# Performance work log

Measured on AMD Instinct MI355X. Metric: run time of the kernel, lower is better.

## Reference

```python
import jax, jax.numpy as jnp
import numpy as np

DIM = 128


def setup_inputs() -> dict:
    key = jax.random.key(0)
    k1, k2, k3, k4 = jax.random.split(key, 4)
    x = jax.random.normal(k1, (8, 32768, DIM), dtype=jnp.float32)
    # nn.Linear(dim, dim*3, bias=False): weight applied as x @ W.T; store as [dim, 3*dim]
    W_qkv = jax.random.normal(k2, (DIM, 3 * DIM), dtype=jnp.float32) * (DIM ** -0.5)
    W_out = jax.random.normal(k3, (DIM, DIM), dtype=jnp.float32) * (DIM ** -0.5)
    b_out = jax.random.normal(k4, (DIM,), dtype=jnp.float32) * 0.01
    return {"x": x, "W_qkv": W_qkv, "W_out": W_out, "b_out": b_out}


def reference(x, W_qkv, W_out, b_out):
    dim = x.shape[-1]
    scale = dim ** -0.5
    qkv = x @ W_qkv  # [b, n, 3d]
    q, k, v = jnp.split(qkv, 3, axis=-1)
    q = jax.nn.softmax(q, axis=-1) * scale
    k = jax.nn.softmax(k, axis=-1)
    v = jax.nn.softmax(v, axis=-1)
    context = jnp.einsum('bnd,bne->bde', q, k)  # [b, d, d]
    out = jnp.einsum('bde,bne->bnd', context, v)  # [b, n, d]
    return out @ W_out + b_out
```

## Files before the change

kernel.cpp:

```cpp
#include <hip/hip_runtime.h>

#define SEQ 32768
#define QSCALE 0.08838834764831845f
#define NCH 16

typedef __attribute__((ext_vector_type(8))) short short8;
typedef __attribute__((ext_vector_type(8))) __bf16 bf16x8;
typedef __attribute__((ext_vector_type(16))) float f32x16;
typedef __attribute__((ext_vector_type(4))) float f32x4;
typedef __attribute__((ext_vector_type(2))) float f32x2;
typedef __attribute__((ext_vector_type(4))) int int4v;
typedef __attribute__((ext_vector_type(2))) int int2v;

#define SWZ(r, c) ((((r) << 7) + (c)) ^ (((r) & 15) << 3))
#define PSWZ(ch, n) ((((ch) << 6) + (n)) ^ (((ch) & 7) << 3))

__device__ __forceinline__ int cvtpk(float lo, float hi) {
  int r;
  asm("v_cvt_pk_bf16_f32 %0, %1, %2" : "=v"(r) : "v"(lo), "v"(hi));
  return r;
}

__device__ __forceinline__ short bf16b(float f) {
  unsigned u = __builtin_bit_cast(unsigned, f);
  u += 0x7fffu + ((u >> 16) & 1u);
  return (short)(u >> 16);
}

__device__ __forceinline__ f32x16 mfma_ii(int4v a, int4v b, f32x16 c) {
  return __builtin_amdgcn_mfma_f32_32x32x16_bf16(
      __builtin_bit_cast(bf16x8, a), __builtin_bit_cast(bf16x8, b), c, 0, 0, 0);
}

__device__ __forceinline__ int4v build_frag(float e0, float e1, float e2, float e3,
                                            float e4, float e5, float e6, float e7,
                                            int hi) {
  int t0 = cvtpk(e0, e1), t1 = cvtpk(e2, e3);
  int t2 = cvtpk(e4, e5), t3 = cvtpk(e6, e7);
  const int u0 = __shfl_xor(t2, 32), u1 = __shfl_xor(t3, 32);
  const int u2 = __shfl_xor(t0, 32), u3 = __shfl_xor(t1, 32);
  int4v f;
  f[0] = hi ? u0 : t0;
  f[1] = hi ? u1 : t1;
  f[2] = hi ? t2 : u2;
  f[3] = hi ? t3 : u3;
  return f;
}

__global__ void la_prep(const float* __restrict__ Wqkv, int4v* __restrict__ Wf) {
  const int fid = blockIdx.x * 256 + threadIdx.x;
  if (fid >= 6144) return;
  const int side = fid >> 11;
  const int rem = fid & 2047;
  const int tile = rem >> 9;
  const int ks = (rem >> 6) & 7;
  const int lane = rem & 63;
  const int k0 = ks * 16 + ((lane >> 5) << 3);
  const int col = side * 128 + tile * 32 + (lane & 31);
  int4v f;
  #pragma unroll
  for (int a = 0; a < 4; ++a)
    f[a] = cvtpk(Wqkv[(k0 + 2 * a) * 384 + col], Wqkv[(k0 + 2 * a + 1) * 384 + col]);
  Wf[fid] = f;
}

__global__ __launch_bounds__(1024, 4)
void la_pass1(const float* __restrict__ x, const int4v* __restrict__ Wf,
              float* __restrict__ partials) {
  __shared__ __align__(16) short xs[2][64 * 128];
  __shared__ __align__(16) short ptile[2][2][128 * 64];
  __shared__ __align__(16) float sumbuf[2][2][2][32][4];

  const int tid = threadIdx.x;
  const int lane = tid & 63;
  const int wv = tid >> 6;
  const int l31 = lane & 31;
  const int hi = lane >> 5;
  const int koff = hi << 3;
  const int h = wv >> 3;
  const int c = (wv >> 1) & 3;
  const int rh = wv & 1;
  const int td = wv >> 2;
  const int te = wv & 3;
  const int b = blockIdx.x >> 5;
  const int strip = blockIdx.x & 31;
  const long base = (long)b * SEQ + (long)strip * (NCH * 64);

  int4v wf[8];
  #pragma unroll
  for (int ks = 0; ks < 8; ++ks)
    wf[ks] = Wf[((((h << 2) + c) << 3) + ks) * 64 + lane];

  const int lr = tid >> 4;
  const int cf = (tid & 15) << 3;
  {
    const float* xp = x + (base + lr) * 128 + cf;
    f32x4 u0 = *(const f32x4*)xp;
    f32x4 u1 = *(const f32x4*)(xp + 4);
    int4v p;
    p[0] = cvtpk(u0[0], u0[1]); p[1] = cvtpk(u0[2], u0[3]);
    p[2] = cvtpk(u1[0], u1[1]); p[3] = cvtpk(u1[2], u1[3]);
    *(int4v*)&xs[0][SWZ(lr, cf)] = p;
  }
  __syncthreads();

  f32x16 ctx = {0.f};
  const int r0 = rh << 5;
  for (int i = 0; i < NCH; ++i) {
    const int cur = i & 1;
    const int inx = (i + 1 < NCH) ? i + 1 : i;
    const float* xp = x + (base + inx * 64 + lr) * 128 + cf;
    f32x4 u0 = *(const f32x4*)xp;
    f32x4 u1 = *(const f32x4*)(xp + 4);

    f32x16 acc = {0.f};
    #pragma unroll
    for (int ks = 0; ks < 8; ++ks) {
      const int4v xf = *(const int4v*)&xs[cur][SWZ(r0 + l31, (ks << 4) + koff)];
      acc = mfma_ii(wf[ks], xf, acc);
    }
    {
      float sa = 0.f, sb = 0.f;
      #pragma unroll
      for (int r = 0; r < 16; r += 2) {
        acc[r] = __expf(acc[r]);         sa += acc[r];
        acc[r + 1] = __expf(acc[r + 1]); sb += acc[r + 1];
      }
      float s = sa + sb;
      s += __shfl_xor(s, 32);
      if (!hi) sumbuf[cur][h][rh][l31][c] = s;
    }

    {
      int4v p;
      p[0] = cvtpk(u0[0], u0[1]); p[1] = cvtpk(u0[2], u0[3]);
      p[2] = cvtpk(u1[0], u1[1]); p[3] = cvtpk(u1[2], u1[3]);
      *(int4v*)&xs[cur ^ 1][SWZ(lr, cf)] = p;
    }
    __syncthreads();

    if (i > 0) {
      const int pb = cur ^ 1;
      #pragma unroll
      for (int ks = 0; ks < 4; ++ks) {
        const int4v aq = *(const int4v*)&ptile[pb][0][PSWZ((td << 5) + l31, (ks << 4) + koff)];
        const int4v bk = *(const int4v*)&ptile[pb][1][PSWZ((te << 5) + l31, (ks << 4) + koff)];
        ctx = mfma_ii(aq, bk, ctx);
      }
    }

    {
      short* pt = &ptile[cur][h][0];
      const int n = (rh << 5) + l31;
      if (h == 0) {
        const f32x4 sq = *(const f32x4*)&sumbuf[cur][0][rh][l31][0];
        const f32x4 sk = *(const f32x4*)&sumbuf[cur][1][rh][l31][0];
        const float invn = QSCALE * __builtin_amdgcn_rcpf(
            (sq[0] + sq[1] + sq[2] + sq[3]) * (sk[0] + sk[1] + sk[2] + sk[3]));
        #pragma unroll
        for (int r = 0; r < 16; ++r) {
          const int ch = (c << 5) + (r & 3) + ((r >> 2) << 3) + (hi << 2);
          pt[PSWZ(ch, n)] = bf16b(acc[r] * invn);
        }
      } else {
        #pragma unroll
        for (int r = 0; r < 16; ++r) {
          const int ch = (c << 5) + (r & 3) + ((r >> 2) << 3) + (hi << 2);
          pt[PSWZ(ch, n)] = bf16b(acc[r]);
        }
      }
    }
  }
  __syncthreads();
  {
    const int pb = (NCH - 1) & 1;
    #pragma unroll
    for (int ks = 0; ks < 4; ++ks) {
      const int4v aq = *(const int4v*)&ptile[pb][0][PSWZ((td << 5) + l31, (ks << 4) + koff)];
      const int4v bk = *(const int4v*)&ptile[pb][1][PSWZ((te << 5) + l31, (ks << 4) + koff)];
      ctx = mfma_ii(aq, bk, ctx);
    }
  }

  float* pout = partials + (long)blockIdx.x * 16384;
  #pragma unroll
  for (int r = 0; r < 16; ++r) {
    const int drow = (td << 5) + (r & 3) + ((r >> 2) << 3) + (hi << 2);
    pout[(drow << 7) + (te << 5) + l31] = ctx[r];
  }
}

__global__ __launch_bounds__(1024, 1)
void la_rm(const float* __restrict__ partials, const float* __restrict__ Wout,
           int4v* __restrict__ Mtf, int strips) {
  __shared__ __align__(16) float cl[128 * 68];
  __shared__ __align__(16) float wo[128 * 128];

  const int tid = threadIdx.x;
  const int b = blockIdx.x >> 1;
  const int eh = blockIdx.x & 1;
  const int ebase = eh << 6;

  #pragma unroll
  for (int t = 0; t < 2; ++t) {
    const int flat = t * 4096 + tid * 4;
    const int d = flat >> 6;
    const int e = flat & 63;
    const long gidx = ((long)d << 7) + ebase + e;
    f32x4 acc = {0.f};
    for (int st = 0; st < strips; ++st)
      acc += *(const f32x4*)(partials + (((long)(b * strips + st)) << 14) + gidx);
    *(f32x4*)&cl[d * 68 + e] = acc;
  }
  #pragma unroll
  for (int t = 0; t < 4; ++t) {
    const int i = t * 4096 + tid * 4;
    *(f32x4*)&wo[i] = *(const f32x4*)(Wout + i);
  }
  __syncthreads();

  const int dq = tid >> 3;
  const int e0 = (tid & 7) << 3;
  float acc[8];
  #pragma unroll
  for (int i = 0; i < 8; ++i) acc[i] = 0.f;
  for (int d = 0; d < 128; ++d) {
    const float w = wo[(d << 7) + dq];
    const float* cr = &cl[d * 68 + e0];
    #pragma unroll
    for (int i = 0; i < 8; ++i) acc[i] += cr[i] * w;
  }

  const int e0g = ebase + e0;
  const int half = dq >> 6, jj = dq & 1, ll = (dq >> 1) & 31;
  const int ks = e0g >> 4, sub = (e0g >> 3) & 1;
  int4v pk;
  pk[0] = cvtpk(acc[0], acc[1]);
  pk[1] = cvtpk(acc[2], acc[3]);
  pk[2] = cvtpk(acc[4], acc[5]);
  pk[3] = cvtpk(acc[6], acc[7]);
  int4v* dst = Mtf + (long)b * 2048 + half * 1024 + jj * 512 + ks * 64;
  dst[sub * 32 + ll] = pk;
}

__global__ __launch_bounds__(256, 4)
void la_pass2(const float* __restrict__ x, const int4v* __restrict__ Wf,
              const int4v* __restrict__ Mtf, const float* __restrict__ bout,
              float* __restrict__ out) {
  __shared__ __align__(16) short xs[4][32 * 128];

  const int tid = threadIdx.x;
  const int lane = tid & 63;
  const int wv = tid >> 6;
  const int l31 = lane & 31;
  const int hi = lane >> 5;
  const int koff = hi << 3;
  const int b = blockIdx.x >> 8;
  const int chunk = blockIdx.x & 255;
  const long row0 = (long)b * SEQ + (long)chunk * 128 + (wv << 5);

  {
    const float* xb = x + row0 * 128;
    f32x4 uA[8];
    #pragma unroll
    for (int t = 0; t < 8; ++t)
      uA[t] = *(const f32x4*)(xb + t * 256 + lane * 4);
    f32x4 uB[8];
    #pragma unroll
    for (int t = 0; t < 8; ++t)
      uB[t] = *(const f32x4*)(xb + (t + 8) * 256 + lane * 4);
    #pragma unroll
    for (int t = 0; t < 8; ++t) {
      const int flat = t * 256 + lane * 4;
      int2v w;
      w[0] = cvtpk(uA[t][0], uA[t][1]);
      w[1] = cvtpk(uA[t][2], uA[t][3]);
      *(int2v*)&xs[wv][SWZ(flat >> 7, flat & 127)] = w;
    }
    #pragma unroll
    for (int t = 0; t < 8; ++t) {
      const int flat = (t + 8) * 256 + lane * 4;
      int2v w;
      w[0] = cvtpk(uB[t][0], uB[t][1]);
      w[1] = cvtpk(uB[t][2], uB[t][3]);
      *(int2v*)&xs[wv][SWZ(flat >> 7, flat & 127)] = w;
    }
  }
  const f32x2 bA = *(const f32x2*)(bout + (l31 << 1));
  const f32x2 bB = *(const f32x2*)(bout + 64 + (l31 << 1));
  asm volatile("s_waitcnt lgkmcnt(0)" ::: "memory");
  __builtin_amdgcn_sched_barrier(0);

  int4v xfr[8];
  #pragma unroll
  for (int ks = 0; ks < 8; ++ks)
    xfr[ks] = *(const int4v*)&xs[wv][SWZ(l31, (ks << 4) + koff)];

  const int4v* WvT = Wf + 2 * 2048;
  f32x16 a0 = {0.f}, a1 = {0.f}, a2 = {0.f}, a3 = {0.f};
  #pragma unroll
  for (int ks = 0; ks < 8; ++ks) {
    a0 = mfma_ii(WvT[(0 * 8 + ks) * 64 + lane], xfr[ks], a0);
    a1 = mfma_ii(WvT[(1 * 8 + ks) * 64 + lane], xfr[ks], a1);
    a2 = mfma_ii(WvT[(2 * 8 + ks) * 64 + lane], xfr[ks], a2);
    a3 = mfma_ii(WvT[(3 * 8 + ks) * 64 + lane], xfr[ks], a3);
  }

  float s = 0.f;
  #pragma unroll
  for (int r = 0; r < 16; ++r) {
    a0[r] = __expf(a0[r]); s += a0[r];
    a1[r] = __expf(a1[r]); s += a1[r];
    a2[r] = __expf(a2[r]); s += a2[r];
    a3[r] = __expf(a3[r]); s += a3[r];
  }
  s += __shfl_xor(s, 32);
  const float inv = __builtin_amdgcn_rcpf(s);
  #pragma unroll
  for (int r = 0; r < 16; ++r) {
    a0[r] *= inv; a1[r] *= inv; a2[r] *= inv; a3[r] *= inv;
  }

  const int4v* MtB = Mtf + ((long)b << 11);
  float* obase = out + row0 * 128 + (l31 << 1);
#define OUT_T2(BASE, T, AT, O0, O1)                                            \
  {                                                                            \
    const int4v f0 = build_frag(AT[0], AT[1], AT[2], AT[3],                    \
                                AT[4], AT[5], AT[6], AT[7], hi);               \
    O0 = mfma_ii(f0, MtB[(BASE) + (2 * T) * 64 + lane], O0);                   \
    O1 = mfma_ii(f0, MtB[(BASE) + 512 + (2 * T) * 64 + lane], O1);             \
    const int4v f1 = build_frag(AT[8], AT[9], AT[10], AT[11],                  \
                                AT[12], AT[13], AT[14], AT[15], hi);           \
    O0 = mfma_ii(f1, MtB[(BASE) + (2 * T + 1) * 64 + lane], O0);               \
    O1 = mfma_ii(f1, MtB[(BASE) + 512 + (2 * T + 1) * 64 + lane], O1);         \
  }
  {
    f32x16 o0 = {0.f}, o1 = {0.f};
    OUT_T2(0, 0, a0, o0, o1)
    OUT_T2(0, 1, a1, o0, o1)
    OUT_T2(0, 2, a2, o0, o1)
    OUT_T2(0, 3, a3, o0, o1)
    #pragma unroll
    for (int r = 0; r < 16; ++r) {
      const int n = (r & 3) + ((r >> 2) << 3) + (hi << 2);
      f32x2 v;
      v[0] = o0[r] + bA[0];
      v[1] = o1[r] + bA[1];
      *(f32x2*)(obase + (long)n * 128) = v;
    }
  }
  {
    f32x16 o2 = {0.f}, o3 = {0.f};
    OUT_T2(1024, 0, a0, o2, o3)
    OUT_T2(1024, 1, a1, o2, o3)
    OUT_T2(1024, 2, a2, o2, o3)
    OUT_T2(1024, 3, a3, o2, o3)
    #pragma unroll
    for (int r = 0; r < 16; ++r) {
      const int n = (r & 3) + ((r >> 2) << 3) + (hi << 2);
      f32x2 v;
      v[0] = o2[r] + bB[0];
      v[1] = o3[r] + bB[1];
      *(f32x2*)(obase + 64 + (long)n * 128) = v;
    }
  }
#undef OUT_T2
}

extern "C" void kernel_launch(void* const* d_in, const int* in_sizes, int n_in,
                              void* d_out, int out_size, void* d_ws, size_t ws_size,
                              hipStream_t stream) {
  const float* x = (const float*)d_in[0];
  const float* Wqkv = (const float*)d_in[1];
  const float* Wout = (const float*)d_in[2];
  const float* bout = (const float*)d_in[3];
  float* out = (float*)d_out;

  const int strips = 32;

  float* partials = (float*)d_ws;
  int4v* Mtf = (int4v*)(partials + (size_t)8 * strips * 16384);
  int4v* Wf = Mtf + 16384;

  la_prep<<<dim3(24), dim3(256), 0, stream>>>(Wqkv, Wf);
  la_pass1<<<dim3(8 * strips), dim3(1024), 0, stream>>>(x, Wf, partials);
  la_rm<<<dim3(16), dim3(1024), 0, stream>>>(partials, Wout, Mtf, strips);
  la_pass2<<<dim3(2048), dim3(256), 0, stream>>>(x, Wf, Mtf, bout, out);
}
```

Before: 144.3 us.

## Compute transposed projection via second MFMA and store prebuilt fragments in LDS

Each wave now runs a second MFMA with swapped operands to get the projection in transposed layout. That layout can be packed straight into MFMA operand fragments with build_frag and stored as whole int4v vectors in LDS, replacing sixteen scattered 16-bit swizzled stores per lane. The original orientation is still computed for the softmax row sums, and the per-row normalisation moves to cross-lane shuffles. This doubles the projection MFMA work to remove the scalar LDS scatter and the bf16 rounding arithmetic in the inner loop.

Result: slower. 157.8 us (+9.3%).

```diff
diff --git a/kernel.cpp b/kernel.cpp
--- a/kernel.cpp
+++ b/kernel.cpp
@@ -13,18 +13,11 @@
 typedef __attribute__((ext_vector_type(2))) int int2v;
 
 #define SWZ(r, c) ((((r) << 7) + (c)) ^ (((r) & 15) << 3))
-#define PSWZ(ch, n) ((((ch) << 6) + (n)) ^ (((ch) & 7) << 3))
 
 __device__ __forceinline__ int cvtpk(float lo, float hi) {
   int r;
   asm("v_cvt_pk_bf16_f32 %0, %1, %2" : "=v"(r) : "v"(lo), "v"(hi));
   return r;
-}
-
-__device__ __forceinline__ short bf16b(float f) {
-  unsigned u = __builtin_bit_cast(unsigned, f);
-  u += 0x7fffu + ((u >> 16) & 1u);
-  return (short)(u >> 16);
 }
 
 __device__ __forceinline__ f32x16 mfma_ii(int4v a, int4v b, f32x16 c) {
@@ -68,7 +61,7 @@
 void la_pass1(const float* __restrict__ x, const int4v* __restrict__ Wf,
               float* __restrict__ partials) {
   __shared__ __align__(16) short xs[2][64 * 128];
-  __shared__ __align__(16) short ptile[2][2][128 * 64];
+  __shared__ int4v fragbuf[2][2][4][4][64];
   __shared__ __align__(16) float sumbuf[2][2][2][32][4];
 
   const int tid = threadIdx.x;
@@ -113,23 +106,26 @@
     f32x4 u0 = *(const f32x4*)xp;
     f32x4 u1 = *(const f32x4*)(xp + 4);
 
-    f32x16 acc = {0.f};
+    f32x16 p2 = {0.f}, p1 = {0.f};
     #pragma unroll
     for (int ks = 0; ks < 8; ++ks) {
       const int4v xf = *(const int4v*)&xs[cur][SWZ(r0 + l31, (ks << 4) + koff)];
-      acc = mfma_ii(wf[ks], xf, acc);
+      p2 = mfma_ii(wf[ks], xf, p2);
+      p1 = mfma_ii(xf, wf[ks], p1);
     }
     {
       float sa = 0.f, sb = 0.f;
       #pragma unroll
       for (int r = 0; r < 16; r += 2) {
-        acc[r] = __expf(acc[r]);         sa += acc[r];
-        acc[r + 1] = __expf(acc[r + 1]); sb += acc[r + 1];
+        sa += __expf(p2[r]);
+        sb += __expf(p2[r + 1]);
       }
       float s = sa + sb;
       s += __shfl_xor(s, 32);
       if (!hi) sumbuf[cur][h][rh][l31][c] = s;
     }
+    #pragma unroll
+    for (int r = 0; r < 16; ++r) p1[r] = __expf(p1[r]);
 
     {
       int4v p;
@@ -142,44 +138,32 @@
     if (i > 0) {
       const int pb = cur ^ 1;
       #pragma unroll
-      for (int ks = 0; ks < 4; ++ks) {
-        const int4v aq = *(const int4v*)&ptile[pb][0][PSWZ((td << 5) + l31, (ks << 4) + koff)];
-        const int4v bk = *(const int4v*)&ptile[pb][1][PSWZ((te << 5) + l31, (ks << 4) + koff)];
-        ctx = mfma_ii(aq, bk, ctx);
+      for (int ks = 0; ks < 4; ++ks)
+        ctx = mfma_ii(fragbuf[pb][0][td][ks][lane], fragbuf[pb][1][te][ks][lane], ctx);
+    }
+
+    if (h == 0) {
+      const f32x4 sq = *(const f32x4*)&sumbuf[cur][0][rh][l31][0];
+      const f32x4 sk = *(const f32x4*)&sumbuf[cur][1][rh][l31][0];
+      const float invn = QSCALE * __builtin_amdgcn_rcpf(
+          (sq[0] + sq[1] + sq[2] + sq[3]) * (sk[0] + sk[1] + sk[2] + sk[3]));
+      #pragma unroll
+      for (int r = 0; r < 16; ++r) {
+        const int nsrc = (r & 3) + ((r >> 2) << 3) + (hi << 2);
+        p1[r] *= __shfl(invn, nsrc);
       }
     }
-
-    {
-      short* pt = &ptile[cur][h][0];
-      const int n = (rh << 5) + l31;
-      if (h == 0) {
-        const f32x4 sq = *(const f32x4*)&sumbuf[cur][0][rh][l31][0];
-        const f32x4 sk = *(const f32x4*)&sumbuf[cur][1][rh][l31][0];
-        const float invn = QSCALE * __builtin_amdgcn_rcpf(
-            (sq[0] + sq[1] + sq[2] + sq[3]) * (sk[0] + sk[1] + sk[2] + sk[3]));
-        #pragma unroll
-        for (int r = 0; r < 16; ++r) {
-          const int ch = (c << 5) + (r & 3) + ((r >> 2) << 3) + (hi << 2);
-          pt[PSWZ(ch, n)] = bf16b(acc[r] * invn);
-        }
-      } else {
-        #pragma unroll
-        for (int r = 0; r < 16; ++r) {
-          const int ch = (c << 5) + (r & 3) + ((r >> 2) << 3) + (hi << 2);
-          pt[PSWZ(ch, n)] = bf16b(acc[r]);
-        }
-      }
-    }
+    fragbuf[cur][h][c][(rh << 1) + 0][lane] =
+        build_frag(p1[0], p1[1], p1[2], p1[3], p1[4], p1[5], p1[6], p1[7], hi);
+    fragbuf[cur][h][c][(rh << 1) + 1][lane] =
+        build_frag(p1[8], p1[9], p1[10], p1[11], p1[12], p1[13], p1[14], p1[15], hi);
   }
   __syncthreads();
   {
     const int pb = (NCH - 1) & 1;
     #pragma unroll
-    for (int ks = 0; ks < 4; ++ks) {
-      const int4v aq = *(const int4v*)&ptile[pb][0][PSWZ((td << 5) + l31, (ks << 4) + koff)];
-      const int4v bk = *(const int4v*)&ptile[pb][1][PSWZ((te << 5) + l31, (ks << 4) + koff)];
-      ctx = mfma_ii(aq, bk, ctx);
-    }
+    for (int ks = 0; ks < 4; ++ks)
+      ctx = mfma_ii(fragbuf[pb][0][td][ks][lane], fragbuf[pb][1][te][ks][lane], ctx);
   }
 
   float* pout = partials + (long)blockIdx.x * 16384;
```
